# Kernel optimization log

Measured on AMD Instinct MI355X. Metric: run time of the kernel, lower is better.

Reference implementation:

```python
import math
import jax, jax.numpy as jnp
import numpy as np

D_MODEL = 1024
HID = 128
H, NB = 16, 16


def setup_inputs() -> dict:
    key = jax.random.key(0)
    ks = jax.random.split(key, 8)
    B, L = 4, 4096
    theta_path = jax.random.normal(ks[0], (B, L, H, NB), dtype=jnp.float32)
    content_emb = jax.random.normal(ks[1], (B, L, D_MODEL), dtype=jnp.float32)
    # measure_head params (PyTorch Linear default init: U(-1/sqrt(fan_in), 1/sqrt(fan_in)))
    s1 = 1.0 / math.sqrt(D_MODEL)
    s2 = 1.0 / math.sqrt(HID)
    W1 = jax.random.uniform(ks[2], (D_MODEL, HID), minval=-s1, maxval=s1, dtype=jnp.float32)
    b1 = jax.random.uniform(ks[3], (HID,), minval=-s1, maxval=s1, dtype=jnp.float32)
    W2 = jax.random.uniform(ks[4], (HID, H * NB), minval=-s2, maxval=s2, dtype=jnp.float32)
    b2 = jax.random.uniform(ks[5], (H * NB,), minval=-s2, maxval=s2, dtype=jnp.float32)
    log_Pi = jnp.zeros((H, NB), dtype=jnp.float32)
    log_R = jnp.zeros((H, NB), dtype=jnp.float32)
    return {"theta_path": theta_path, "content_emb": content_emb, "W1": W1, "b1": b1,
            "W2": W2, "b2": b2, "log_Pi": log_Pi, "log_R": log_R}


def _affine_scan(alpha, u):
    # d_t = alpha_t * d_{t-1} + u_t, d_0 = u_0 (zero initial state), scan over axis=1 (L)
    def combine(left, right):
        a_l, u_l = left
        a_r, u_r = right
        return a_l * a_r, a_r * u_l + u_r
    _, d = jax.lax.associative_scan(combine, (alpha, u), axis=1)
    return d


def reference(theta_path, content_emb, W1, b1, W2, b2, log_Pi, log_R):
    B, L, _, _ = theta_path.shape
    h = jax.nn.gelu(content_emb @ W1 + b1, approximate=False)  # [B,L,128], exact GELU as torch
    z = jnp.pi * jnp.tanh((h @ W2 + b2).reshape(B, L, H, NB))
    diff = z - theta_path
    nu = jnp.arctan2(jnp.sin(diff), jnp.cos(diff))  # wrapped angle residual
    Pi = jnp.exp(log_Pi)[None, None]  # [1,1,H,NB]
    R = jnp.exp(log_R)[None, None]
    K = Pi / jnp.maximum(Pi + R, 1e-08)
    Kf = jnp.broadcast_to(K, (B, L, H, NB))
    alpha = 1.0 - Kf
    u = Kf * nu
    d = _affine_scan(alpha, u)
    return (theta_path + d,
            jnp.broadcast_to(Pi, (B, L, H, NB)),
            Kf,
            jnp.broadcast_to(R, (B, L, H, NB)))
```

## Files before the change

kernel.cpp:

```cpp
#include <hip/hip_runtime.h>
#include <math.h>

#define MTOT  16384
#define DM    1024
#define HIDN  128
#define HNB   256
#define NBAT  4
#define CLK   64
#define NBLK  256
#define CPB   64

typedef _Float16 v8h __attribute__((ext_vector_type(8)));
typedef float    v4f __attribute__((ext_vector_type(4)));
#define MFMA16(a,b,c) __builtin_amdgcn_mfma_f32_16x16x32_f16((a),(b),(c),0,0,0)

#define W1BLOB_TILE 20480
#define W2BLOB_BASE 655360
#define W2BLOB_TILE 40960
#define BLOB_BYTES  819200

#define KEEPF4(v) asm volatile("" : "+v"((v).x), "+v"((v).y), "+v"((v).z), "+v"((v).w))
#define KEEPI4(v) asm volatile("" : "+v"((v).x), "+v"((v).y), "+v"((v).z), "+v"((v).w))

#define BAR_LGKM() do { \
    asm volatile("s_waitcnt lgkmcnt(0)" ::: "memory"); \
    __builtin_amdgcn_s_barrier(); \
    __builtin_amdgcn_sched_barrier(0); \
} while (0)

union U16 { int4 i; v8h h; };

__device__ __forceinline__ void cvt_store(float4 v, char* ph, char* pl) {
    union { _Float16 h[4]; int2 i; } H, L;
    float a[4] = {v.x, v.y, v.z, v.w};
    #pragma unroll
    for (int e = 0; e < 4; ++e) {
        _Float16 hh = (_Float16)a[e];
        H.h[e] = hh;
        L.h[e] = (_Float16)((a[e] - (float)hh) * 4096.f);
    }
    *(int2*)ph = H.i;
    *(int2*)pl = L.i;
}

__global__ __launch_bounds__(256) void k_prep(
    const float* __restrict__ W1,
    const float* __restrict__ W2,
    char* __restrict__ blobs)
{
    __shared__ float lds[32][260];
    const int t = threadIdx.x, blk = blockIdx.x;
    if (blk < 32) {
        const int k0 = blk * 32;
        #pragma unroll
        for (int i = 0; i < 4; ++i) {
            int j = t + i * 256;
            int k = j >> 5, n4 = (j & 31) << 2;
            *(float4*)&lds[k][n4] = *(const float4*)&W1[(size_t)(k0 + k) * HIDN + n4];
        }
        __syncthreads();
        const int n = t >> 1, kh = t & 1;
        union { _Float16 h[16]; int2 v[4]; } uh, ul;
        #pragma unroll
        for (int kk = 0; kk < 16; ++kk) {
            float v = lds[kh * 16 + kk][n];
            _Float16 hh = (_Float16)v;
            uh.h[kk] = hh;
            ul.h[kk] = (_Float16)((v - (float)hh) * 4096.f);
        }
        char* bh = blobs + blk * W1BLOB_TILE + n * 80 + kh * 32;
        #pragma unroll
        for (int i = 0; i < 4; ++i) {
            *(int2*)(bh + i * 8)         = uh.v[i];
            *(int2*)(bh + 10240 + i * 8) = ul.v[i];
        }
        if (kh == 1) {
            int2 z; z.x = 0; z.y = 0;
            char* ph = blobs + blk * W1BLOB_TILE + n * 80 + 64;
            *(int2*)(ph) = z; *(int2*)(ph + 8) = z;
            *(int2*)(ph + 10240) = z; *(int2*)(ph + 10240 + 8) = z;
        }
    } else {
        const int ks = blk - 32, k0 = ks * 32;
        #pragma unroll
        for (int i = 0; i < 8; ++i) {
            int j = t + i * 256;
            int k = j >> 6, n4 = (j & 63) << 2;
            *(float4*)&lds[k][n4] = *(const float4*)&W2[(size_t)(k0 + k) * HNB + n4];
        }
        __syncthreads();
        const int n = t;
        union { _Float16 h[40]; int2 v[10]; } uh, ul;
        #pragma unroll
        for (int kk = 0; kk < 32; ++kk) {
            float v = lds[kk][n];
            _Float16 hh = (_Float16)v;
            uh.h[kk] = hh;
            ul.h[kk] = (_Float16)((v - (float)hh) * 4096.f);
        }
        #pragma unroll
        for (int kk = 32; kk < 40; ++kk) { uh.h[kk] = (_Float16)0.f; ul.h[kk] = (_Float16)0.f; }
        char* bh = blobs + W2BLOB_BASE + ks * W2BLOB_TILE + n * 80;
        #pragma unroll
        for (int i = 0; i < 10; ++i) {
            *(int2*)(bh + i * 8)         = uh.v[i];
            *(int2*)(bh + 20480 + i * 8) = ul.v[i];
        }
    }
}

__global__ __launch_bounds__(512, 2) void k_mega(
    const float* __restrict__ A,
    const float* __restrict__ theta,
    const float* __restrict__ b1, const float* __restrict__ b2,
    const float* __restrict__ logPi, const float* __restrict__ logR,
    const char* __restrict__ blobs,
    float* __restrict__ out0, float* __restrict__ out2,
    float* fill1, float* fill3,
    float* carry, int cstride)
{
    __shared__ __attribute__((aligned(16))) char smem[67584];

    const int tid  = threadIdx.x;
    const int blk  = blockIdx.x;
    const int m0   = blk * CLK;
    const int lane = tid & 63;
    const int wid  = tid >> 6;
    const int ln15 = lane & 15;
    const int q    = lane >> 4;
    const int np1  = wid & 3;
    const int gk   = wid >> 2;

    const int srow = tid >> 3;
    const int skq  = (tid & 7) * 4;
    const int wby  = srow * 64 + (((skq >> 3) ^ ((srow >> 1) & 3)) << 4) + ((skq >> 2) & 1) * 8;
    const float* aBase = A + (size_t)(m0 + srow) * DM + skq;

    int aby[4];
    #pragma unroll
    for (int mi = 0; mi < 4; ++mi) {
        int row = 16 * mi + ln15;
        aby[mi] = row * 64 + ((q ^ ((row >> 1) & 3)) << 4);
    }

    const char* wb[2];
    wb[0] = blobs + (32 * np1 + ln15) * 80 + q * 16;
    wb[1] = blobs + (32 * np1 + 16 + ln15) * 80 + q * 16;

    v4f acc1[4][2], acc2[4][2];
    #pragma unroll
    for (int mi = 0; mi < 4; ++mi)
        #pragma unroll
        for (int ni = 0; ni < 2; ++ni) {
            acc1[mi][ni] = (v4f){0.f, 0.f, 0.f, 0.f};
            acc2[mi][ni] = (v4f){0.f, 0.f, 0.f, 0.f};
        }

    {
        float4 u0 = *(const float4*)(aBase);
        float4 u1 = *(const float4*)(aBase + 16 * 32);
        cvt_store(u0, smem + wby,        smem + 16384 + wby);
        cvt_store(u1, smem + 4096 + wby, smem + 16384 + 4096 + wby);
    }
    float4 ra[4][2];
    #pragma unroll
    for (int s = 0; s < 4; ++s) {
        ra[s][0] = *(const float4*)(aBase + (size_t)(1 + s) * 32);
        ra[s][1] = *(const float4*)(aBase + (size_t)(17 + s) * 32);
        KEEPF4(ra[s][0]); KEEPF4(ra[s][1]);
    }
    int4 cwh[2], cwl[2];
    #pragma unroll
    for (int ni = 0; ni < 2; ++ni) {
        const char* p = wb[ni] + (size_t)(gk * 16) * W1BLOB_TILE;
        cwh[ni] = *(const int4*)(p);
        cwl[ni] = *(const int4*)(p + 10240);
        KEEPI4(cwh[ni]); KEEPI4(cwl[ni]);
    }
    BAR_LGKM();

    for (int jo = 0; jo < 4; ++jo) {
        #pragma unroll
        for (int j2 = 0; j2 < 4; ++j2) {
            const int j = jo * 4 + j2;
            const int p = j2 & 1;
            const bool more = (jo < 3) || (j2 < 3);
            if (more) {
                const int sp = p ^ 1;
                cvt_store(ra[j2][0], smem + (sp * 2 + 0) * 4096 + wby,
                                     smem + 16384 + (sp * 2 + 0) * 4096 + wby);
                cvt_store(ra[j2][1], smem + (sp * 2 + 1) * 4096 + wby,
                                     smem + 16384 + (sp * 2 + 1) * 4096 + wby);
                if (j + 5 <= 15) {
                    ra[j2][0] = *(const float4*)(aBase + (size_t)(j + 5) * 32);
                    ra[j2][1] = *(const float4*)(aBase + (size_t)(j + 21) * 32);
                    KEEPF4(ra[j2][0]); KEEPF4(ra[j2][1]);
                }
            }
            int4 nwh[2], nwl[2];
            if (more) {
                #pragma unroll
                for (int ni = 0; ni < 2; ++ni) {
                    const char* pw = wb[ni] + (size_t)(gk * 16 + j + 1) * W1BLOB_TILE;
                    nwh[ni] = *(const int4*)(pw);
                    nwl[ni] = *(const int4*)(pw + 10240);
                    KEEPI4(nwh[ni]); KEEPI4(nwl[ni]);
                }
            }
            const char* ab = smem + (p * 2 + gk) * 4096;
            v8h ah[4], al[4];
            #pragma unroll
            for (int mi = 0; mi < 4; ++mi) {
                ah[mi] = *(const v8h*)(ab + aby[mi]);
                al[mi] = *(const v8h*)(ab + 16384 + aby[mi]);
            }
            U16 h0, h1, l0, l1;
            h0.i = cwh[0]; h1.i = cwh[1]; l0.i = cwl[0]; l1.i = cwl[1];
            #pragma unroll
            for (int mi = 0; mi < 4; ++mi) {
                acc1[mi][0] = MFMA16(ah[mi], h0.h, acc1[mi][0]);
                acc2[mi][0] = MFMA16(ah[mi], l0.h, acc2[mi][0]);
                acc2[mi][0] = MFMA16(al[mi], h0.h, acc2[mi][0]);
                acc1[mi][1] = MFMA16(ah[mi], h1.h, acc1[mi][1]);
                acc2[mi][1] = MFMA16(ah[mi], l1.h, acc2[mi][1]);
                acc2[mi][1] = MFMA16(al[mi], h1.h, acc2[mi][1]);
            }
            if (more) {
                cwh[0] = nwh[0]; cwh[1] = nwh[1];
                cwl[0] = nwl[0]; cwl[1] = nwl[1];
            }
            BAR_LGKM();
        }
    }

    const float inv = 1.f / 4096.f;
    if (gk == 1) {
        #pragma unroll
        for (int mi = 0; mi < 4; ++mi)
            #pragma unroll
            for (int ni = 0; ni < 2; ++ni)
                #pragma unroll
                for (int r = 0; r < 4; ++r) {
                    int row = 16 * mi + 4 * q + r;
                    int col = 32 * np1 + 16 * ni + ln15;
                    *(float*)(smem + row * 512 + col * 4) =
                        acc1[mi][ni][r] + acc2[mi][ni][r] * inv;
                }
    }
    BAR_LGKM();
    if (gk == 0) {
        #pragma unroll
        for (int mi = 0; mi < 4; ++mi)
            #pragma unroll
            for (int ni = 0; ni < 2; ++ni) {
                int col = 32 * np1 + 16 * ni + ln15;
                float bv = b1[col];
                #pragma unroll
                for (int r = 0; r < 4; ++r) {
                    int row = 16 * mi + 4 * q + r;
                    float y = acc1[mi][ni][r] + acc2[mi][ni][r] * inv
                            + *(const float*)(smem + row * 512 + col * 4) + bv;
                    float h = 0.5f * y * (1.f + erff(y * 0.70710678118654752f));
                    _Float16 hh = (_Float16)h;
                    _Float16 hl = (_Float16)((h - (float)hh) * 4096.f);
                    int byte_ = row * 272 + ((((col >> 3) ^ ((row >> 1) & 3))) << 4)
                              + (col & 7) * 2;
                    *(_Float16*)(smem + 32768 + byte_) = hh;
                    *(_Float16*)(smem + 50176 + byte_) = hl;
                }
            }
    }
    BAR_LGKM();

    v4f c1[4][2], c2[4][2];
    #pragma unroll
    for (int mi = 0; mi < 4; ++mi)
        #pragma unroll
        for (int ni = 0; ni < 2; ++ni) {
            c1[mi][ni] = (v4f){0.f, 0.f, 0.f, 0.f};
            c2[mi][ni] = (v4f){0.f, 0.f, 0.f, 0.f};
        }
    const char* w2b[2];
    w2b[0] = blobs + W2BLOB_BASE + (32 * wid + ln15) * 80 + q * 16;
    w2b[1] = blobs + W2BLOB_BASE + (32 * wid + 16 + ln15) * 80 + q * 16;

    #pragma unroll
    for (int ks = 0; ks < 4; ++ks) {
        v8h hh[4], hl[4];
        #pragma unroll
        for (int mi = 0; mi < 4; ++mi) {
            int frow = 16 * mi + ln15;
            int byte_ = frow * 272 + ((4 * ks + (q ^ ((frow >> 1) & 3))) << 4);
            hh[mi] = *(const v8h*)(smem + 32768 + byte_);
            hl[mi] = *(const v8h*)(smem + 50176 + byte_);
        }
        #pragma unroll
        for (int ni = 0; ni < 2; ++ni) {
            U16 wh_, wl_;
            wh_.i = *(const int4*)(w2b[ni] + (size_t)ks * W2BLOB_TILE);
            wl_.i = *(const int4*)(w2b[ni] + (size_t)ks * W2BLOB_TILE + 20480);
            #pragma unroll
            for (int mi = 0; mi < 4; ++mi) {
                c1[mi][ni] = MFMA16(hh[mi], wh_.h, c1[mi][ni]);
                c2[mi][ni] = MFMA16(hh[mi], wl_.h, c2[mi][ni]);
                c2[mi][ni] = MFMA16(hl[mi], wh_.h, c2[mi][ni]);
            }
        }
    }
    BAR_LGKM();

    #pragma unroll
    for (int mi = 0; mi < 4; ++mi)
        #pragma unroll
        for (int ni = 0; ni < 2; ++ni) {
            int col = 32 * wid + 16 * ni + ln15;
            float bv = b2[col];
            #pragma unroll
            for (int r = 0; r < 4; ++r) {
                int row = 16 * mi + 4 * q + r;
                float y2 = c1[mi][ni][r] + c2[mi][ni][r] * inv + bv;
                *(float*)(smem + row * 1040 + col * 4) =
                    3.14159265358979323846f * tanhf(y2);
            }
        }
    BAR_LGKM();

    if (tid < 256) {
        const int c = tid;
        const float Pi = expf(logPi[c]);
        const float Rr = expf(logR[c]);
        const float Kc = Pi / fmaxf(Pi + Rr, 1e-8f);
        const float alpha = 1.f - Kc;
        float d = 0.f;
        float tv[2][16];
        #pragma unroll
        for (int i = 0; i < 16; ++i)
            tv[0][i] = theta[(size_t)(m0 + i) * HNB + c];
        #pragma unroll
        for (int g = 0; g < 4; ++g) {
            const int cur = g & 1;
            if (g < 3) {
                #pragma unroll
                for (int i = 0; i < 16; ++i)
                    tv[cur ^ 1][i] = theta[(size_t)(m0 + (g + 1) * 16 + i) * HNB + c];
            }
            float sv[16];
            #pragma unroll
            for (int i = 0; i < 16; ++i) {
                float z = *(const float*)(smem + (g * 16 + i) * 1040 + c * 4);
                float diff = z - tv[cur][i];
                float kq = rintf(diff * 0.15915494309189533577f);
                float nu = (float)((double)diff - (double)kq * 6.283185307179586476925286766559);
                d = fmaf(alpha, d, Kc * nu);
                sv[i] = tv[cur][i] + d;
            }
            #pragma unroll
            for (int i = 0; i < 16; ++i)
                out0[(size_t)(m0 + g * 16 + i) * HNB + c] = sv[i];
        }
        carry[(size_t)blk * cstride + c] = d;
    } else {
        const int c = tid - 256;
        const float Pi = expf(logPi[c]);
        const float Rr = expf(logR[c]);
        const float Kc = Pi / fmaxf(Pi + Rr, 1e-8f);
        if (fill1) {
            #pragma unroll 4
            for (int i = 0; i < CLK; ++i) {
                size_t idx = (size_t)(m0 + i) * HNB + c;
                out2[idx]  = Kc;
                fill1[idx] = Pi;
                fill3[idx] = Rr;
            }
        } else {
            #pragma unroll 4
            for (int i = 0; i < CLK; ++i)
                out2[(size_t)(m0 + i) * HNB + c] = Kc;
        }
    }
}

__global__ __launch_bounds__(256) void k_cscan(
    const float* __restrict__ logPi, const float* __restrict__ logR,
    float* carry, int cstride, int crep)
{
    const int c = threadIdx.x, b = blockIdx.x;
    const float Pi = expf(logPi[c]);
    const float Rr = expf(logR[c]);
    const float alpha = 1.f - Pi / fmaxf(Pi + Rr, 1e-8f);
    float A64 = alpha;
    #pragma unroll
    for (int i = 0; i < 6; ++i) A64 *= A64;
    float D = 0.f;
    for (int s0 = 0; s0 < CPB; s0 += 16) {
        float a[16];
        #pragma unroll
        for (int j = 0; j < 16; ++j)
            a[j] = carry[(size_t)(b * CPB + s0 + j) * cstride + c];
        #pragma unroll
        for (int j = 0; j < 16; ++j) {
            size_t base = (size_t)(b * CPB + s0 + j) * cstride;
            carry[base + c]        = D;
            carry[base + crep + c] = D;
            D = fmaf(A64, D, a[j]);
        }
    }
}

__global__ __launch_bounds__(256) void k_apply(
    const float* __restrict__ logPi, const float* __restrict__ logR,
    float* __restrict__ out0, float* out1, float* out3,
    const float* carry, int cstride, int crep, int do_fills)
{
    const int blk = blockIdx.x;
    const int chunk = blk >> 1, half = blk & 1;
    const int c = threadIdx.x;
    const float Pi = expf(logPi[c]);
    const float Rr = expf(logR[c]);
    const float Kc = Pi / fmaxf(Pi + Rr, 1e-8f);
    const float alpha = 1.f - Kc;
    float D = carry[(size_t)chunk * cstride + (size_t)half * crep + c];
    float w = alpha * D;
    if (half) {
        float a32 = alpha;
        #pragma unroll
        for (int i = 0; i < 5; ++i) a32 *= a32;
        w *= a32;
    }
    const size_t base = (size_t)chunk * (CLK * HNB) + (size_t)half * (32 * HNB) + c;
    if (do_fills) {
        #pragma unroll 4
        for (int i = 0; i < 32; ++i) {
            size_t idx = base + (size_t)i * HNB;
            out0[idx] += w;
            out1[idx] = Pi;
            out3[idx] = Rr;
            w *= alpha;
        }
    } else {
        #pragma unroll 4
        for (int i = 0; i < 32; ++i) {
            size_t idx = base + (size_t)i * HNB;
            out0[idx] += w;
            w *= alpha;
        }
    }
}

extern "C" void kernel_launch(void* const* d_in, const int* in_sizes, int n_in,
                              void* d_out, int out_size, void* d_ws, size_t ws_size,
                              hipStream_t stream) {
    const float* theta   = (const float*)d_in[0];
    const float* content = (const float*)d_in[1];
    const float* W1      = (const float*)d_in[2];
    const float* b1      = (const float*)d_in[3];
    const float* W2      = (const float*)d_in[4];
    const float* b2      = (const float*)d_in[5];
    const float* logPi   = (const float*)d_in[6];
    const float* logR    = (const float*)d_in[7];

    float* out  = (float*)d_out;
    float* out0 = out;
    float* out1 = out + (size_t)MTOT * HNB;
    float* out2 = out + (size_t)2 * MTOT * HNB;
    float* out3 = out + (size_t)3 * MTOT * HNB;

    const size_t carry_bytes = (size_t)NBLK * 512 * 4;
    const size_t need = carry_bytes + BLOB_BYTES;
    float* carry; int cstride, crep, do_fills; char* blobs;
    float *f1, *f3;
    if (ws_size >= need) {
        carry   = (float*)d_ws;
        cstride = 512; crep = 256;
        blobs   = (char*)d_ws + carry_bytes;
        f1 = out1; f3 = out3; do_fills = 0;
    } else {
        carry   = out3;
        cstride = 16384; crep = 8192;
        blobs   = (char*)out1;
        f1 = nullptr; f3 = nullptr; do_fills = 1;
    }

    hipLaunchKernelGGL(k_prep, dim3(36), dim3(256), 0, stream, W1, W2, blobs);
    hipLaunchKernelGGL(k_mega, dim3(NBLK), dim3(512), 0, stream,
                       content, theta, b1, b2, logPi, logR, blobs,
                       out0, out2, f1, f3, carry, cstride);
    hipLaunchKernelGGL(k_cscan, dim3(NBAT), dim3(256), 0, stream,
                       logPi, logR, carry, cstride, crep);
    hipLaunchKernelGGL(k_apply, dim3(NBLK * 2), dim3(256), 0, stream,
                       logPi, logR, out0, out1, out3, carry, cstride, crep, do_fills);
}
```

Before: 71.18 us.

## Stage A and weight tiles via global_load_lds async copies with double buffering

Replaces register-staged global loads of the activation and W1/W2 weight tiles with direct global-to-LDS async loads (global_load_lds), double-buffered and synchronised with vmcnt waits. The fp32 A tile lands raw in LDS and is then split into fp16 hi/lo parts from LDS. W2 tiles are also prefetched into LDS while the GELU epilogue runs. LDS use grows to about 146 KB, which may cut occupancy below the two blocks per CU the launch bounds request.

New measurement: 59.35 us. -16.6%, faster.

```diff
diff --git a/kernel.cpp b/kernel.cpp
--- a/kernel.cpp
+++ b/kernel.cpp
@@ -12,6 +12,7 @@
 
 typedef _Float16 v8h __attribute__((ext_vector_type(8)));
 typedef float    v4f __attribute__((ext_vector_type(4)));
+typedef int      v4i __attribute__((ext_vector_type(4)));
 #define MFMA16(a,b,c) __builtin_amdgcn_mfma_f32_16x16x32_f16((a),(b),(c),0,0,0)
 
 #define W1BLOB_TILE 20480
@@ -19,28 +20,40 @@
 #define W2BLOB_TILE 40960
 #define BLOB_BYTES  819200
 
-#define KEEPF4(v) asm volatile("" : "+v"((v).x), "+v"((v).y), "+v"((v).z), "+v"((v).w))
-#define KEEPI4(v) asm volatile("" : "+v"((v).x), "+v"((v).y), "+v"((v).z), "+v"((v).w))
-
-#define BAR_LGKM() do { \
-    asm volatile("s_waitcnt lgkmcnt(0)" ::: "memory"); \
-    __builtin_amdgcn_s_barrier(); \
-    __builtin_amdgcn_sched_barrier(0); \
-} while (0)
-
-union U16 { int4 i; v8h h; };
-
-__device__ __forceinline__ void cvt_store(float4 v, char* ph, char* pl) {
-    union { _Float16 h[4]; int2 i; } H, L;
-    float a[4] = {v.x, v.y, v.z, v.w};
+#define RAW0   0
+#define AH0    32768
+#define AL0    49152
+#define W1L    65536
+#define YOFF   0
+#define HH0    32768
+#define HL0    50176
+#define W2L    67584
+#define ZOFF   0
+#define SMEMSZ 149504
+
+#define VMCNT(N) asm volatile("s_waitcnt vmcnt(" #N ")" ::: "memory")
+#define BARRIER() do { asm volatile("s_waitcnt lgkmcnt(0)" ::: "memory"); \
+                       __builtin_amdgcn_s_barrier(); } while (0)
+
+typedef const __attribute__((address_space(1))) void* gas1_t;
+typedef __attribute__((address_space(3))) void* las3_t;
+
+__device__ __forceinline__ void gld16(const void* g, void* l) {
+    __builtin_amdgcn_global_load_lds((gas1_t)g, (las3_t)l, 16, 0, 0);
+}
+
+__device__ __forceinline__ void split8(v4f a, v4f b, v4i* H, v4i* L) {
+    union { _Float16 h[8]; v4i v; } hh, ll;
     #pragma unroll
     for (int e = 0; e < 4; ++e) {
-        _Float16 hh = (_Float16)a[e];
-        H.h[e] = hh;
-        L.h[e] = (_Float16)((a[e] - (float)hh) * 4096.f);
-    }
-    *(int2*)ph = H.i;
-    *(int2*)pl = L.i;
+        _Float16 t0 = (_Float16)a[e];
+        hh.h[e] = t0;
+        ll.h[e] = (_Float16)((a[e] - (float)t0) * 4096.f);
+        _Float16 t1 = (_Float16)b[e];
+        hh.h[e + 4] = t1;
+        ll.h[e + 4] = (_Float16)((b[e] - (float)t1) * 4096.f);
+    }
+    *H = hh.v; *L = ll.v;
 }
 
 __global__ __launch_bounds__(256) void k_prep(
@@ -119,7 +132,7 @@
     float* fill1, float* fill3,
     float* carry, int cstride)
 {
-    __shared__ __attribute__((aligned(16))) char smem[67584];
+    __shared__ __attribute__((aligned(16))) char smem[SMEMSZ];
 
     const int tid  = threadIdx.x;
     const int blk  = blockIdx.x;
@@ -131,10 +144,23 @@
     const int np1  = wid & 3;
     const int gk   = wid >> 2;
 
-    const int srow = tid >> 3;
-    const int skq  = (tid & 7) * 4;
-    const int wby  = srow * 64 + (((skq >> 3) ^ ((srow >> 1) & 3)) << 4) + ((skq >> 2) & 1) * 8;
-    const float* aBase = A + (size_t)(m0 + srow) * DM + skq;
+    const int rowoff0 = (wid & 3) * 16 + (lane >> 3);
+    const int rowoff1 = rowoff0 + 8;
+    const int swf = ((lane & 7) ^ (lane >> 3)) * 4;
+    const float* aSrc0 = A + (size_t)(m0 + rowoff0) * DM + (size_t)(wid >> 2) * 512 + swf;
+    const float* aSrc1 = A + (size_t)(m0 + rowoff1) * DM + (size_t)(wid >> 2) * 512 + swf;
+    const int rawDst = (wid >> 2) * 8192 + (wid & 3) * 2048;
+
+    const int crow = (wid & 3) * 16 + (lane >> 2);
+    const int cseg = lane & 3;
+    const int cvtRowOff = (wid >> 2) * 8192 + crow * 128;
+    const int rb0 = ((2 * cseg)     ^ (crow & 7)) * 16;
+    const int rb1 = ((2 * cseg + 1) ^ (crow & 7)) * 16;
+    const int wbyC = crow * 64 + ((cseg ^ ((crow >> 1) & 3)) << 4);
+    const int sh = wid >> 2;
+
+    const char* wSrc = blobs + (size_t)(wid >> 2) * 16 * W1BLOB_TILE
+                     + (size_t)(wid & 3) * 5120 + (size_t)lane * 16;
 
     int aby[4];
     #pragma unroll
@@ -143,10 +169,6 @@
         aby[mi] = row * 64 + ((q ^ ((row >> 1) & 3)) << 4);
     }
 
-    const char* wb[2];
-    wb[0] = blobs + (32 * np1 + ln15) * 80 + q * 16;
-    wb[1] = blobs + (32 * np1 + 16 + ln15) * 80 + q * 16;
-
     v4f acc1[4][2], acc2[4][2];
     #pragma unroll
     for (int mi = 0; mi < 4; ++mi)
@@ -156,121 +178,117 @@
             acc2[mi][ni] = (v4f){0.f, 0.f, 0.f, 0.f};
         }
 
+    gld16(aSrc0, smem + RAW0 + rawDst);
+    gld16(aSrc1, smem + RAW0 + rawDst + 1024);
+    #pragma unroll
+    for (int i = 0; i < 5; ++i)
+        gld16(wSrc + i * 1024, smem + W1L + wid * 5120 + i * 1024);
+    gld16(aSrc0 + 32, smem + RAW0 + 16384 + rawDst);
+    gld16(aSrc1 + 32, smem + RAW0 + 16384 + rawDst + 1024);
+    VMCNT(7);
     {
-        float4 u0 = *(const float4*)(aBase);
-        float4 u1 = *(const float4*)(aBase + 16 * 32);
-        cvt_store(u0, smem + wby,        smem + 16384 + wby);
-        cvt_store(u1, smem + 4096 + wby, smem + 16384 + 4096 + wby);
-    }
-    float4 ra[4][2];
-    #pragma unroll
-    for (int s = 0; s < 4; ++s) {
-        ra[s][0] = *(const float4*)(aBase + (size_t)(1 + s) * 32);
-        ra[s][1] = *(const float4*)(aBase + (size_t)(17 + s) * 32);
-        KEEPF4(ra[s][0]); KEEPF4(ra[s][1]);
-    }
-    int4 cwh[2], cwl[2];
-    #pragma unroll
-    for (int ni = 0; ni < 2; ++ni) {
-        const char* p = wb[ni] + (size_t)(gk * 16) * W1BLOB_TILE;
-        cwh[ni] = *(const int4*)(p);
-        cwl[ni] = *(const int4*)(p + 10240);
-        KEEPI4(cwh[ni]); KEEPI4(cwl[ni]);
-    }
-    BAR_LGKM();
-
-    for (int jo = 0; jo < 4; ++jo) {
-        #pragma unroll
-        for (int j2 = 0; j2 < 4; ++j2) {
-            const int j = jo * 4 + j2;
-            const int p = j2 & 1;
-            const bool more = (jo < 3) || (j2 < 3);
-            if (more) {
-                const int sp = p ^ 1;
-                cvt_store(ra[j2][0], smem + (sp * 2 + 0) * 4096 + wby,
-                                     smem + 16384 + (sp * 2 + 0) * 4096 + wby);
-                cvt_store(ra[j2][1], smem + (sp * 2 + 1) * 4096 + wby,
-                                     smem + 16384 + (sp * 2 + 1) * 4096 + wby);
-                if (j + 5 <= 15) {
-                    ra[j2][0] = *(const float4*)(aBase + (size_t)(j + 5) * 32);
-                    ra[j2][1] = *(const float4*)(aBase + (size_t)(j + 21) * 32);
-                    KEEPF4(ra[j2][0]); KEEPF4(ra[j2][1]);
+        const char* rb = smem + RAW0 + cvtRowOff;
+        v4f r0 = *(const v4f*)(rb + rb0);
+        v4f r1 = *(const v4f*)(rb + rb1);
+        v4i Hq, Lq; split8(r0, r1, &Hq, &Lq);
+        *(v4i*)(smem + AH0 + sh * 8192 + wbyC) = Hq;
+        *(v4i*)(smem + AL0 + sh * 8192 + wbyC) = Lq;
+    }
+    VMCNT(2);
+    BARRIER();
+
+    #pragma unroll
+    for (int kt = 0; kt < 16; ++kt) {
+        const int buf = kt & 1, nb = buf ^ 1;
+        if (kt < 15) {
+            const char* ws = wSrc + (size_t)(kt + 1) * W1BLOB_TILE;
+            char* wd = smem + W1L + nb * 40960 + wid * 5120;
+            #pragma unroll
+            for (int i = 0; i < 5; ++i) gld16(ws + i * 1024, wd + i * 1024);
+        }
+        if (kt < 14) {
+            char* rd = smem + RAW0 + buf * 16384 + rawDst;
+            gld16(aSrc0 + (size_t)(kt + 2) * 32, rd);
+            gld16(aSrc1 + (size_t)(kt + 2) * 32, rd + 1024);
+        }
+        {
+            const char* abH = smem + AH0 + gk * 8192 + buf * 4096;
+            const char* abL = smem + AL0 + gk * 8192 + buf * 4096;
+            const char* wb  = smem + W1L + buf * 40960 + gk * 20480;
+            v8h ah[4], al[4];
+            #pragma unroll
+            for (int mi = 0; mi < 4; ++mi) {
+                ah[mi] = *(const v8h*)(abH + aby[mi]);
+                al[mi] = *(const v8h*)(abL + aby[mi]);
+            }
+            #pragma unroll
+            for (int ni = 0; ni < 2; ++ni) {
+                const int wo = (32 * np1 + 16 * ni + ln15) * 80 + q * 16;
+                v8h wfh = *(const v8h*)(wb + wo);
+                v8h wfl = *(const v8h*)(wb + 10240 + wo);
+                #pragma unroll
+                for (int mi = 0; mi < 4; ++mi) {
+                    acc1[mi][ni] = MFMA16(ah[mi], wfh, acc1[mi][ni]);
+                    acc2[mi][ni] = MFMA16(ah[mi], wfl, acc2[mi][ni]);
+                    acc2[mi][ni] = MFMA16(al[mi], wfh, acc2[mi][ni]);
                 }
             }
-            int4 nwh[2], nwl[2];
-            if (more) {
-                #pragma unroll
-                for (int ni = 0; ni < 2; ++ni) {
-                    const char* pw = wb[ni] + (size_t)(gk * 16 + j + 1) * W1BLOB_TILE;
-                    nwh[ni] = *(const int4*)(pw);
-                    nwl[ni] = *(const int4*)(pw + 10240);
-                    KEEPI4(nwh[ni]); KEEPI4(nwl[ni]);
-                }
-            }
-            const char* ab = smem + (p * 2 + gk) * 4096;
-            v8h ah[4], al[4];
-            #pragma unroll
-            for (int mi = 0; mi < 4; ++mi) {
-                ah[mi] = *(const v8h*)(ab + aby[mi]);
-                al[mi] = *(const v8h*)(ab + 16384 + aby[mi]);
-            }
-            U16 h0, h1, l0, l1;
-            h0.i = cwh[0]; h1.i = cwh[1]; l0.i = cwl[0]; l1.i = cwl[1];
-            #pragma unroll
-            for (int mi = 0; mi < 4; ++mi) {
-                acc1[mi][0] = MFMA16(ah[mi], h0.h, acc1[mi][0]);
-                acc2[mi][0] = MFMA16(ah[mi], l0.h, acc2[mi][0]);
-                acc2[mi][0] = MFMA16(al[mi], h0.h, acc2[mi][0]);
-                acc1[mi][1] = MFMA16(ah[mi], h1.h, acc1[mi][1]);
-                acc2[mi][1] = MFMA16(ah[mi], l1.h, acc2[mi][1]);
-                acc2[mi][1] = MFMA16(al[mi], h1.h, acc2[mi][1]);
-            }
-            if (more) {
-                cwh[0] = nwh[0]; cwh[1] = nwh[1];
-                cwl[0] = nwl[0]; cwl[1] = nwl[1];
-            }
-            BAR_LGKM();
-        }
-    }
+        }
+        if (kt < 15) {
+            if (kt < 14) { VMCNT(7); } else { VMCNT(5); }
+            const char* rb = smem + RAW0 + nb * 16384 + cvtRowOff;
+            v4f r0 = *(const v4f*)(rb + rb0);
+            v4f r1 = *(const v4f*)(rb + rb1);
+            v4i Hq, Lq; split8(r0, r1, &Hq, &Lq);
+            *(v4i*)(smem + AH0 + sh * 8192 + nb * 4096 + wbyC) = Hq;
+            *(v4i*)(smem + AL0 + sh * 8192 + nb * 4096 + wbyC) = Lq;
+        }
+        if (kt < 14) { VMCNT(2); }
+        else if (kt == 14) { VMCNT(0); }
+        BARRIER();
+    }
+
+    const char* w2Src = blobs + W2BLOB_BASE + (size_t)wid * 5120 + (size_t)lane * 16;
+    #pragma unroll
+    for (int i = 0; i < 5; ++i)
+        gld16(w2Src + i * 1024, smem + W2L + wid * 5120 + i * 1024);
 
     const float inv = 1.f / 4096.f;
     if (gk == 1) {
         #pragma unroll
         for (int mi = 0; mi < 4; ++mi)
             #pragma unroll
-            for (int ni = 0; ni < 2; ++ni)
+            for (int ni = 0; ni < 2; ++ni) {
+                v4f y = acc1[mi][ni] + acc2[mi][ni] * inv;
+                *(v4f*)(smem + YOFF + np1 * 8192 + (mi * 2 + ni) * 1024 + lane * 16) = y;
+            }
+    }
+    BARRIER();
+    if (gk == 0) {
+        #pragma unroll
+        for (int mi = 0; mi < 4; ++mi)
+            #pragma unroll
+            for (int ni = 0; ni < 2; ++ni) {
+                v4f yo = *(const v4f*)(smem + YOFF + np1 * 8192 + (mi * 2 + ni) * 1024 + lane * 16);
+                const int col = 32 * np1 + 16 * ni + ln15;
+                const float bv = b1[col];
                 #pragma unroll
                 for (int r = 0; r < 4; ++r) {
-                    int row = 16 * mi + 4 * q + r;
-                    int col = 32 * np1 + 16 * ni + ln15;
-                    *(float*)(smem + row * 512 + col * 4) =
-                        acc1[mi][ni][r] + acc2[mi][ni][r] * inv;
+                    float y = acc1[mi][ni][r] + acc2[mi][ni][r] * inv + yo[r] + bv;
+                    float h = 0.5f * y * (1.f + erff(y * 0.70710678118654752f));
+                    _Float16 hh2 = (_Float16)h;
+                    _Float16 hl2 = (_Float16)((h - (float)hh2) * 4096.f);
+                    const int row = 16 * mi + 4 * q + r;
+                    const int byte_ = row * 272 + ((((col >> 3) ^ ((row >> 1) & 3))) << 4)
+                                    + (col & 7) * 2;
+                    *(_Float16*)(smem + HH0 + byte_) = hh2;
+                    *(_Float16*)(smem + HL0 + byte_) = hl2;
                 }
-    }
-    BAR_LGKM();
-    if (gk == 0) {
-        #pragma unroll
-        for (int mi = 0; mi < 4; ++mi)
-            #pragma unroll
-            for (int ni = 0; ni < 2; ++ni) {
-                int col = 32 * np1 + 16 * ni + ln15;
-                float bv = b1[col];
-                #pragma unroll
-                for (int r = 0; r < 4; ++r) {
-                    int row = 16 * mi + 4 * q + r;
-                    float y = acc1[mi][ni][r] + acc2[mi][ni][r] * inv
-                            + *(const float*)(smem + row * 512 + col * 4) + bv;
-                    float h = 0.5f * y * (1.f + erff(y * 0.70710678118654752f));
-                    _Float16 hh = (_Float16)h;
-                    _Float16 hl = (_Float16)((h - (float)hh) * 4096.f);
-                    int byte_ = row * 272 + ((((col >> 3) ^ ((row >> 1) & 3))) << 4)
-                              + (col & 7) * 2;
-                    *(_Float16*)(smem + 32768 + byte_) = hh;
-                    *(_Float16*)(smem + 50176 + byte_) = hl;
-                }
-            }
-    }
-    BAR_LGKM();
+            }
+    }
+    BARRIER();
+    VMCNT(0);
+    BARRIER();
 
     v4f c1[4][2], c2[4][2];
     #pragma unroll
@@ -280,34 +298,38 @@
             c1[mi][ni] = (v4f){0.f, 0.f, 0.f, 0.f};
             c2[mi][ni] = (v4f){0.f, 0.f, 0.f, 0.f};
         }
-    const char* w2b[2];
-    w2b[0] = blobs + W2BLOB_BASE + (32 * wid + ln15) * 80 + q * 16;
-    w2b[1] = blobs + W2BLOB_BASE + (32 * wid + 16 + ln15) * 80 + q * 16;
-
     #pragma unroll
     for (int ks = 0; ks < 4; ++ks) {
+        if (ks < 3) {
+            const char* ws = w2Src + (size_t)(ks + 1) * W2BLOB_TILE;
+            char* wd = smem + W2L + ((ks + 1) & 1) * 40960 + wid * 5120;
+            #pragma unroll
+            for (int i = 0; i < 5; ++i) gld16(ws + i * 1024, wd + i * 1024);
+        }
+        const char* w2b = smem + W2L + (ks & 1) * 40960;
         v8h hh[4], hl[4];
         #pragma unroll
         for (int mi = 0; mi < 4; ++mi) {
             int frow = 16 * mi + ln15;
-            int byte_ = frow * 272 + ((4 * ks + (q ^ ((frow >> 1) & 3))) << 4);
-            hh[mi] = *(const v8h*)(smem + 32768 + byte_);
-            hl[mi] = *(const v8h*)(smem + 50176 + byte_);
+            int hby = frow * 272 + ((4 * ks + (q ^ ((frow >> 1) & 3))) << 4);
+            hh[mi] = *(const v8h*)(smem + HH0 + hby);
+            hl[mi] = *(const v8h*)(smem + HL0 + hby);
         }
         #pragma unroll
         for (int ni = 0; ni < 2; ++ni) {
-            U16 wh_, wl_;
-            wh_.i = *(const int4*)(w2b[ni] + (size_t)ks * W2BLOB_TILE);
-            wl_.i = *(const int4*)(w2b[ni] + (size_t)ks * W2BLOB_TILE + 20480);
+            const int wo2 = (32 * wid + 16 * ni + ln15) * 80 + q * 16;
+            v8h w2h = *(const v8h*)(w2b + wo2);
+            v8h w2l = *(const v8h*)(w2b + 20480 + wo2);
             #pragma unroll
             for (int mi = 0; mi < 4; ++mi) {
-                c1[mi][ni] = MFMA16(hh[mi], wh_.h, c1[mi][ni]);
-                c2[mi][ni] = MFMA16(hh[mi], wl_.h, c2[mi][ni]);
-                c2[mi][ni] = MFMA16(hl[mi], wh_.h, c2[mi][ni]);
-            }
-        }
-    }
-    BAR_LGKM();
+                c1[mi][ni] = MFMA16(hh[mi], w2h, c1[mi][ni]);
+                c2[mi][ni] = MFMA16(hh[mi], w2l, c2[mi][ni]);
+                c2[mi][ni] = MFMA16(hl[mi], w2h, c2[mi][ni]);
+            }
+        }
+        VMCNT(0);
+        BARRIER();
+    }
 
     #pragma unroll
     for (int mi = 0; mi < 4; ++mi)
@@ -319,11 +341,11 @@
             for (int r = 0; r < 4; ++r) {
                 int row = 16 * mi + 4 * q + r;
                 float y2 = c1[mi][ni][r] + c2[mi][ni][r] * inv + bv;
-                *(float*)(smem + row * 1040 + col * 4) =
+                *(float*)(smem + ZOFF + row * 1040 + col * 4) =
                     3.14159265358979323846f * tanhf(y2);
             }
         }
-    BAR_LGKM();
+    BARRIER();
 
     if (tid < 256) {
         const int c = tid;
@@ -347,7 +369,7 @@
             float sv[16];
             #pragma unroll
             for (int i = 0; i < 16; ++i) {
-                float z = *(const float*)(smem + (g * 16 + i) * 1040 + c * 4);
+                float z = *(const float*)(smem + ZOFF + (g * 16 + i) * 1040 + c * 4);
                 float diff = z - tv[cur][i];
                 float kq = rintf(diff * 0.15915494309189533577f);
                 float nu = (float)((double)diff - (double)kq * 6.283185307179586476925286766559);
```
